# Performance work log

Hardware: AMD Instinct MI355X
Metric: run time of the kernel (lower is better)

The kernel has to match this reference:

```python
import jax, jax.numpy as jnp
import numpy as np

IN, HID, OUT = 512, 2048, 128
B, T = 8, 512


def setup_inputs() -> dict:
    key = jax.random.key(0)
    ks = jax.random.split(key, 8)
    k = 1.0 / np.sqrt(HID)  # torch default init scale for RNN/Linear
    u = lambda kk, shape: jax.random.uniform(kk, shape, jnp.float32, -k, k)
    return {
        "x": jax.random.normal(ks[0], (B, T, IN), jnp.float32),
        "W_ih": u(ks[1], (HID, IN)),
        "b_ih": u(ks[2], (HID,)),
        "W_hh": u(ks[3], (HID, HID)),
        "b_hh": u(ks[4], (HID,)),
        "W_out": u(ks[5], (OUT, HID)),
        "b_out": u(ks[6], (OUT,)),
    }


def reference(x, W_ih, b_ih, W_hh, b_hh, W_out, b_out):
    # Pre-project inputs for all timesteps in one big GEMM: [B,T,HID]
    xp = jnp.einsum("bti,hi->bth", x, W_ih) + b_ih + b_hh

    def step(h, xt):  # h: [B,HID], xt: [B,HID]
        h = jnp.tanh(xt + h @ W_hh.T)
        return h, h

    h0 = jnp.zeros((x.shape[0], W_hh.shape[0]), x.dtype)
    _, hs = jax.lax.scan(step, h0, jnp.swapaxes(xp, 0, 1))  # hs: [T,B,HID]
    hs = jnp.swapaxes(hs, 0, 1)  # [B,T,HID]
    return hs @ W_out.T + b_out  # [B,T,OUT]
```

## Files before the change

kernel.cpp:

```cpp
#include <hip/hip_runtime.h>


#define IN_K   512
#define HID    2048
#define OUTN   128
#define BB     8
#define TSTEPS 512
#define NWG    64
#define SENT   0xFF80FF80u

typedef __bf16 bf16x8 __attribute__((ext_vector_type(8)));
typedef unsigned short u16x8 __attribute__((ext_vector_type(8)));
typedef unsigned int u32x4 __attribute__((ext_vector_type(4)));
typedef float f32v4 __attribute__((ext_vector_type(4)));

union Frag8 { u16x8 u; bf16x8 b; u32x4 d; };

__device__ __forceinline__ unsigned short f2bf(float f) {
  unsigned int u = __float_as_uint(f);
  return (unsigned short)((u + 0x7FFFu + ((u >> 16) & 1u)) >> 16);
}

__device__ __forceinline__ float tanh_fast(float x) {
  return 1.0f - 2.0f / (__expf(2.0f * x) + 1.0f);
}

__global__ __launch_bounds__(256)
void sentinel_kernel(u32x4* __restrict__ p) {
  const size_t i = (size_t)blockIdx.x * 256 + threadIdx.x;
  u32x4 v; v[0] = SENT; v[1] = SENT; v[2] = SENT; v[3] = SENT;
  p[i] = v;
}

template<int EPI>
__global__ __launch_bounds__(256, 2)
void gemm_kernel(const void* __restrict__ Aptr, const float* __restrict__ Bptr,
                 const float* __restrict__ bias0, const float* __restrict__ bias1,
                 float* __restrict__ Cout, const int Kdim, const int Ndim)
{
  __shared__ __align__(16) unsigned short As[64][56];
  __shared__ __align__(16) unsigned short Bs[64][56];

  const int m0 = blockIdx.x * 64;
  const int n0 = blockIdx.y * 64;
  const int tid = threadIdx.x;
  const int w = tid >> 6, l = tid & 63;
  const int l15 = l & 15, lk = (l >> 4) * 8;
  const int wm = (w >> 1) * 32, wn = (w & 1) * 32;

  f32v4 acc[2][2];
  #pragma unroll
  for (int mt = 0; mt < 2; ++mt)
    #pragma unroll
    for (int nt = 0; nt < 2; ++nt)
      #pragma unroll
      for (int r = 0; r < 4; ++r) acc[mt][nt][r] = 0.0f;

  for (int k0 = 0; k0 < Kdim; k0 += 32) {
    __syncthreads();
    if (EPI == 0) {
      const float* A = (const float*)Aptr;
      const int r = tid >> 3, c4 = (tid & 7) * 4;
      #pragma unroll
      for (int it = 0; it < 2; ++it) {
        const float4 v = *(const float4*)(A + (size_t)(m0 + r + it * 32) * Kdim + k0 + c4);
        unsigned short* d = &As[r + it * 32][c4];
        d[0] = f2bf(v.x); d[1] = f2bf(v.y); d[2] = f2bf(v.z); d[3] = f2bf(v.w);
      }
    } else {
      const unsigned short* A = (const unsigned short*)Aptr;
      const int r = tid >> 2, c8 = (tid & 3) * 8;
      const u16x8 v = *(const u16x8*)(A + (size_t)(m0 + r) * Kdim + k0 + c8);
      *(u16x8*)&As[r][c8] = v;
    }
    {
      const int r = tid >> 3, c4 = (tid & 7) * 4;
      #pragma unroll
      for (int it = 0; it < 2; ++it) {
        const float4 v = *(const float4*)(Bptr + (size_t)(n0 + r + it * 32) * Kdim + k0 + c4);
        unsigned short* d = &Bs[r + it * 32][c4];
        d[0] = f2bf(v.x); d[1] = f2bf(v.y); d[2] = f2bf(v.z); d[3] = f2bf(v.w);
      }
    }
    __syncthreads();

    Frag8 af[2], bg[2];
    #pragma unroll
    for (int mt = 0; mt < 2; ++mt) af[mt].u = *(const u16x8*)&As[wm + mt * 16 + l15][lk];
    #pragma unroll
    for (int nt = 0; nt < 2; ++nt) bg[nt].u = *(const u16x8*)&Bs[wn + nt * 16 + l15][lk];
    #pragma unroll
    for (int mt = 0; mt < 2; ++mt)
      #pragma unroll
      for (int nt = 0; nt < 2; ++nt)
        acc[mt][nt] = __builtin_amdgcn_mfma_f32_16x16x32_bf16(af[mt].b, bg[nt].b, acc[mt][nt], 0, 0, 0);
  }

  #pragma unroll
  for (int mt = 0; mt < 2; ++mt)
    #pragma unroll
    for (int nt = 0; nt < 2; ++nt)
      #pragma unroll
      for (int r = 0; r < 4; ++r) {
        const int m = m0 + wm + mt * 16 + (l >> 4) * 4 + r;
        const int n = n0 + wn + nt * 16 + l15;
        float v = acc[mt][nt][r];
        if (EPI == 0) {
          v += bias0[n] + bias1[n];
          const int b = m >> 9, t = m & 511;
          Cout[((size_t)t * BB + b) * Ndim + n] = v;
        } else {
          v += bias0[n];
          Cout[(size_t)m * Ndim + n] = v;
        }
      }
}

__global__ __launch_bounds__(256, 1)
void scan_kernel(const float* __restrict__ Whh, const float* __restrict__ xp,
                 unsigned short* __restrict__ hs)
{
  const int g = blockIdx.x;
  const int tid = threadIdx.x;
  const int w = tid >> 6, l = tid & 63;
  const int l15 = l & 15, lk = (l >> 4) * 8;
  const int jbase = g * 32;

  Frag8 Bw[2][16];
  #pragma unroll
  for (int nt = 0; nt < 2; ++nt) {
    const int j = jbase + nt * 16 + l15;
    #pragma unroll
    for (int kc = 0; kc < 16; ++kc) {
      const int k = w * 512 + kc * 32 + lk;
      const float4* p = (const float4*)(Whh + (size_t)j * HID + k);
      const float4 u0 = p[0], u1 = p[1];
      Frag8 f;
      f.u[0] = f2bf(u0.x); f.u[1] = f2bf(u0.y); f.u[2] = f2bf(u0.z); f.u[3] = f2bf(u0.w);
      f.u[4] = f2bf(u1.x); f.u[5] = f2bf(u1.y); f.u[6] = f2bf(u1.z); f.u[7] = f2bf(u1.w);
      Bw[nt][kc] = f;
    }
  }

  __shared__ float red[4][2][16][16];
  const int om = tid >> 4;
  const int oj2 = (tid & 15) * 2;
  const int half = oj2 >> 4, col = oj2 & 15;
  const int arow = l15 & 7;

  for (int t = 0; t < TSTEPS; ++t) {
    float xv0 = 0.f, xv1 = 0.f;
    if (tid < 128) {
      const float2 xv = *(const float2*)(xp + ((size_t)t * BB + om) * HID + jbase + oj2);
      xv0 = xv.x; xv1 = xv.y;
    }

    f32v4 acc0, acc1;
    #pragma unroll
    for (int r = 0; r < 4; ++r) { acc0[r] = 0.f; acc1[r] = 0.f; }

    if (t > 0) {
      const unsigned short* hb = hs + ((size_t)arow * TSTEPS + (t - 1)) * HID + w * 512 + lk;
      Frag8 a[16];
      while (true) {
        #pragma unroll
        for (int kc = 0; kc < 16; ++kc) {
          asm volatile("global_load_dwordx4 %0, %1, off offset:%2 sc0 sc1"
                       : "=v"(a[kc].d) : "v"(hb), "n"(kc * 64));
        }
        asm volatile("s_waitcnt vmcnt(0)" ::: "memory");
        unsigned int mv = 0xFFFFFFFFu;
        #pragma unroll
        for (int kc = 0; kc < 16; ++kc)
          #pragma unroll
          for (int dwi = 0; dwi < 4; ++dwi)
            mv = min(mv, a[kc].d[dwi] ^ SENT);
        if (__all(mv != 0u)) break;
      }
      __builtin_amdgcn_sched_barrier(0);
      #pragma unroll
      for (int kc = 0; kc < 16; ++kc) {
        acc0 = __builtin_amdgcn_mfma_f32_16x16x32_bf16(a[kc].b, Bw[0][kc].b, acc0, 0, 0, 0);
        acc1 = __builtin_amdgcn_mfma_f32_16x16x32_bf16(a[kc].b, Bw[1][kc].b, acc1, 0, 0, 0);
      }
    }

    #pragma unroll
    for (int r = 0; r < 4; ++r) {
      red[w][0][(l >> 4) * 4 + r][l15] = acc0[r];
      red[w][1][(l >> 4) * 4 + r][l15] = acc1[r];
    }
    __syncthreads();

    if (tid < 128) {
      float s0 = red[0][half][om][col]     + red[1][half][om][col]
               + red[2][half][om][col]     + red[3][half][om][col]     + xv0;
      float s1 = red[0][half][om][col + 1] + red[1][half][om][col + 1]
               + red[2][half][om][col + 1] + red[3][half][om][col + 1] + xv1;
      const float h0 = tanh_fast(s0), h1 = tanh_fast(s1);
      const unsigned int packed = (unsigned int)f2bf(h0) | ((unsigned int)f2bf(h1) << 16);
      unsigned int* hp = (unsigned int*)(hs + ((size_t)om * TSTEPS + t) * HID + jbase + oj2);
      __hip_atomic_store(hp, packed, __ATOMIC_RELAXED, __HIP_MEMORY_SCOPE_AGENT);
    }
    __syncthreads();
  }
}

extern "C" void kernel_launch(void* const* d_in, const int* in_sizes, int n_in,
                              void* d_out, int out_size, void* d_ws, size_t ws_size,
                              hipStream_t stream)
{
  (void)in_sizes; (void)n_in; (void)out_size; (void)ws_size;
  const float* x    = (const float*)d_in[0];
  const float* Wih  = (const float*)d_in[1];
  const float* bih  = (const float*)d_in[2];
  const float* Whh  = (const float*)d_in[3];
  const float* bhh  = (const float*)d_in[4];
  const float* Wout = (const float*)d_in[5];
  const float* bout = (const float*)d_in[6];
  float* out = (float*)d_out;

  char* ws = (char*)d_ws;
  float* xp          = (float*)(ws);
  unsigned short* hs = (unsigned short*)(ws + (size_t)(32 << 20));

  sentinel_kernel<<<dim3(4096), 256, 0, stream>>>((u32x4*)hs);
  gemm_kernel<0><<<dim3(64, 32), 256, 0, stream>>>(x, Wih, bih, bhh, xp, IN_K, HID);
  scan_kernel<<<dim3(NWG), 256, 0, stream>>>(Whh, xp, hs);
  gemm_kernel<1><<<dim3(64, 2), 256, 0, stream>>>(hs, Wout, bout, nullptr, out, HID, OUTN);
}
```

Before: 1.987 ms.

## Replace sentinel-polling sync with per-workgroup step flags in RNN scan

Drops the sentinel fill kernel and the polling of whole h-state tiles for a sentinel value. Each scan workgroup now publishes a step counter flag after storing its slice of h, and consumers spin on the 16 flags covering their K-range before loading h once. The flags are zeroed by the first GEMM kernel. This removes a 16 MB memset and reduces polling traffic, at the cost of an extra store/wait per step and a flag-then-data ordering that relies on the sc0 sc1 stores and loads being coherent.

```diff
diff --git a/kernel.cpp b/kernel.cpp
--- a/kernel.cpp
+++ b/kernel.cpp
@@ -7,11 +7,11 @@
 #define BB     8
 #define TSTEPS 512
 #define NWG    64
-#define SENT   0xFF80FF80u
 
 typedef __bf16 bf16x8 __attribute__((ext_vector_type(8)));
 typedef unsigned short u16x8 __attribute__((ext_vector_type(8)));
 typedef unsigned int u32x4 __attribute__((ext_vector_type(4)));
+typedef int i32x4 __attribute__((ext_vector_type(4)));
 typedef float f32v4 __attribute__((ext_vector_type(4)));
 
 union Frag8 { u16x8 u; bf16x8 b; u32x4 d; };
@@ -23,21 +23,17 @@
 
 __device__ __forceinline__ float tanh_fast(float x) {
   return 1.0f - 2.0f / (__expf(2.0f * x) + 1.0f);
-}
-
-__global__ __launch_bounds__(256)
-void sentinel_kernel(u32x4* __restrict__ p) {
-  const size_t i = (size_t)blockIdx.x * 256 + threadIdx.x;
-  u32x4 v; v[0] = SENT; v[1] = SENT; v[2] = SENT; v[3] = SENT;
-  p[i] = v;
 }
 
 template<int EPI>
 __global__ __launch_bounds__(256, 2)
 void gemm_kernel(const void* __restrict__ Aptr, const float* __restrict__ Bptr,
                  const float* __restrict__ bias0, const float* __restrict__ bias1,
-                 float* __restrict__ Cout, const int Kdim, const int Ndim)
+                 float* __restrict__ Cout, const int Kdim, const int Ndim,
+                 int* __restrict__ bar)
 {
+  if (EPI == 0 && blockIdx.x == 0 && blockIdx.y == 0 && threadIdx.x < 72)
+    bar[threadIdx.x] = 0;
   __shared__ __align__(16) unsigned short As[64][56];
   __shared__ __align__(16) unsigned short Bs[64][56];
 
@@ -118,7 +114,7 @@
 
 __global__ __launch_bounds__(256, 1)
 void scan_kernel(const float* __restrict__ Whh, const float* __restrict__ xp,
-                 unsigned short* __restrict__ hs)
+                 unsigned short* __restrict__ hs, int* __restrict__ bar)
 {
   const int g = blockIdx.x;
   const int tid = threadIdx.x;
@@ -143,10 +139,12 @@
   }
 
   __shared__ float red[4][2][16][16];
+  int* flags = bar + 8;
   const int om = tid >> 4;
   const int oj2 = (tid & 15) * 2;
   const int half = oj2 >> 4, col = oj2 & 15;
   const int arow = l15 & 7;
+  const int* fp = flags + w * 16;
 
   for (int t = 0; t < TSTEPS; ++t) {
     float xv0 = 0.f, xv1 = 0.f;
@@ -160,23 +158,29 @@
     for (int r = 0; r < 4; ++r) { acc0[r] = 0.f; acc1[r] = 0.f; }
 
     if (t > 0) {
+      i32x4 f0, f1, f2, f3;
+      while (true) {
+        asm volatile("global_load_dwordx4 %0, %4, off sc0 sc1\n\t"
+                     "global_load_dwordx4 %1, %4, off offset:16 sc0 sc1\n\t"
+                     "global_load_dwordx4 %2, %4, off offset:32 sc0 sc1\n\t"
+                     "global_load_dwordx4 %3, %4, off offset:48 sc0 sc1"
+                     : "=v"(f0), "=v"(f1), "=v"(f2), "=v"(f3) : "v"(fp));
+        asm volatile("s_waitcnt vmcnt(0)" ::: "memory");
+        __builtin_amdgcn_sched_barrier(0);
+        int mn = min(min(min(f0[0], f0[1]), min(f0[2], f0[3])),
+                     min(min(f1[0], f1[1]), min(f1[2], f1[3])));
+        mn = min(mn, min(min(min(f2[0], f2[1]), min(f2[2], f2[3])),
+                         min(min(f3[0], f3[1]), min(f3[2], f3[3]))));
+        if (mn >= t) break;
+      }
       const unsigned short* hb = hs + ((size_t)arow * TSTEPS + (t - 1)) * HID + w * 512 + lk;
       Frag8 a[16];
-      while (true) {
-        #pragma unroll
-        for (int kc = 0; kc < 16; ++kc) {
-          asm volatile("global_load_dwordx4 %0, %1, off offset:%2 sc0 sc1"
-                       : "=v"(a[kc].d) : "v"(hb), "n"(kc * 64));
-        }
-        asm volatile("s_waitcnt vmcnt(0)" ::: "memory");
-        unsigned int mv = 0xFFFFFFFFu;
-        #pragma unroll
-        for (int kc = 0; kc < 16; ++kc)
-          #pragma unroll
-          for (int dwi = 0; dwi < 4; ++dwi)
-            mv = min(mv, a[kc].d[dwi] ^ SENT);
-        if (__all(mv != 0u)) break;
-      }
+      #pragma unroll
+      for (int kc = 0; kc < 16; ++kc) {
+        asm volatile("global_load_dwordx4 %0, %1, off offset:%2 sc0 sc1"
+                     : "=v"(a[kc].d) : "v"(hb), "n"(kc * 64));
+      }
+      asm volatile("s_waitcnt vmcnt(0)" ::: "memory");
       __builtin_amdgcn_sched_barrier(0);
       #pragma unroll
       for (int kc = 0; kc < 16; ++kc) {
@@ -200,9 +204,15 @@
       const float h0 = tanh_fast(s0), h1 = tanh_fast(s1);
       const unsigned int packed = (unsigned int)f2bf(h0) | ((unsigned int)f2bf(h1) << 16);
       unsigned int* hp = (unsigned int*)(hs + ((size_t)om * TSTEPS + t) * HID + jbase + oj2);
-      __hip_atomic_store(hp, packed, __ATOMIC_RELAXED, __HIP_MEMORY_SCOPE_AGENT);
-    }
-    __syncthreads();
+      asm volatile("global_store_dword %0, %1, off sc0 sc1" :: "v"(hp), "v"(packed) : "memory");
+    }
+    asm volatile("s_waitcnt vmcnt(0)" ::: "memory");
+    __syncthreads();
+    if (tid == 0) {
+      const int fl = t + 1;
+      asm volatile("global_store_dword %0, %1, off sc0 sc1"
+                   :: "v"(&flags[g]), "v"(fl) : "memory");
+    }
   }
 }
 
@@ -223,9 +233,9 @@
   char* ws = (char*)d_ws;
   float* xp          = (float*)(ws);
   unsigned short* hs = (unsigned short*)(ws + (size_t)(32 << 20));
-
-  sentinel_kernel<<<dim3(4096), 256, 0, stream>>>((u32x4*)hs);
-  gemm_kernel<0><<<dim3(64, 32), 256, 0, stream>>>(x, Wih, bih, bhh, xp, IN_K, HID);
-  scan_kernel<<<dim3(NWG), 256, 0, stream>>>(Whh, xp, hs);
-  gemm_kernel<1><<<dim3(64, 2), 256, 0, stream>>>(hs, Wout, bout, nullptr, out, HID, OUTN);
-}
+  int* bar           = (int*)(ws + (size_t)(48 << 20));
+
+  gemm_kernel<0><<<dim3(64, 32), 256, 0, stream>>>(x, Wih, bih, bhh, xp, IN_K, HID, bar);
+  scan_kernel<<<dim3(NWG), 256, 0, stream>>>(Whh, xp, hs, bar);
+  gemm_kernel<1><<<dim3(64, 2), 256, 0, stream>>>(hs, Wout, bout, nullptr, out, HID, OUTN, bar);
+}
```

Measured after the change: 2.701 ms. 1.36x slower.
